# Kernel tuning notes

Measured on AMD Instinct MI355X. Metric: run time of the kernel, lower is better.

## Reference

```python
import jax, jax.numpy as jnp
import numpy as np

B, T, C = 16, 2048, 128
HEAD_SIZE = 128

def setup_inputs() -> dict:
    key = jax.random.key(0)
    k1, k2, k3, k4 = jax.random.split(key, 4)
    x = jax.random.normal(k1, (B, T, C), dtype=jnp.float32)
    # nn.Linear(N_EMBED, head_size, bias=False) weight shape: [head_size, N_EMBED]
    scale = (1.0 / np.sqrt(C)).astype(np.float32)
    Wq = jax.random.normal(k2, (HEAD_SIZE, C), dtype=jnp.float32) * scale
    Wk = jax.random.normal(k3, (HEAD_SIZE, C), dtype=jnp.float32) * scale
    Wv = jax.random.normal(k4, (HEAD_SIZE, C), dtype=jnp.float32) * scale
    return {"x": x, "Wq": Wq, "Wk": Wk, "Wv": Wv}

def reference(x, Wq, Wk, Wv):
    Bd, Td, Cd = x.shape
    q = jnp.einsum('btc,hc->bth', x, Wq)  # [B,T,H]
    k = jnp.einsum('btc,hc->bth', x, Wk)
    v = jnp.einsum('btc,hc->bth', x, Wv)
    # NOTE: original scales by C**-0.5 (embedding dim), not head_size**-0.5
    scores = jnp.einsum('bth,bsh->bts', q, k) * (Cd ** -0.5)  # [B,T,T]
    causal = jnp.tril(jnp.ones((Td, Td), dtype=bool))
    scores = jnp.where(causal, scores, -jnp.inf)
    attn = jax.nn.softmax(scores, axis=-1)
    out = jnp.einsum('bts,bsh->bth', attn, v)  # [B,T,H]
    return out
```

## Files before the change

kernel.cpp:

```cpp
#include <hip/hip_runtime.h>
#include <hip/hip_bf16.h>

#define BB 16
#define TT 2048
#define CC 128
#define HH 128
#define NQT128 16

typedef __bf16 bf16x8 __attribute__((ext_vector_type(8)));
typedef float  f32x4  __attribute__((ext_vector_type(4)));

#define BTH       ((size_t)BB * TT * HH)
#define WBF_OFF   (3 * BTH)
#define PARTIAL_OFF_BYTES (3 * BTH * 2 + 3 * 128 * 128 * 2)
#define SLOT_FLOATS (128 * 128 + 128)

static __device__ __forceinline__ bf16x8 load_cvt8(const float* __restrict__ p) {
    float4 a = *(const float4*)p;
    float4 b = *(const float4*)(p + 4);
    bf16x8 r;
    r[0] = (__bf16)a.x; r[1] = (__bf16)a.y; r[2] = (__bf16)a.z; r[3] = (__bf16)a.w;
    r[4] = (__bf16)b.x; r[5] = (__bf16)b.y; r[6] = (__bf16)b.z; r[7] = (__bf16)b.w;
    return r;
}

static __device__ __forceinline__ void load_lds16(const void* g, void* l) {
    __builtin_amdgcn_global_load_lds(
        (const __attribute__((address_space(1))) unsigned int*)g,
        (__attribute__((address_space(3))) unsigned int*)l, 16, 0, 0);
}

__global__ __launch_bounds__(256) void wcvt_kernel(
    const float* __restrict__ Wq, const float* __restrict__ Wk,
    const float* __restrict__ Wv, __bf16* __restrict__ wbf)
{
    int idx = blockIdx.x * 256 + threadIdx.x;
    int m = idx >> 14;
    int e = idx & 16383;
    const float* src = (m == 0) ? Wq : (m == 1) ? Wk : Wv;
    float sc = (m == 0) ? (0.08838834764831845f * 1.4426950408889634f) : 1.0f;
    wbf[idx] = (__bf16)(src[e] * sc);
}

#define TR_QK 132
#define TR_V  68

__global__ __launch_bounds__(256) void proj_kernel(
    const float* __restrict__ x, __bf16* __restrict__ ws)
{
    __shared__ __bf16 tr[128 * TR_V];

    const int lane = threadIdx.x & 63;
    const int wave = threadIdx.x >> 6;
    const int quad = lane >> 4;
    const int l16  = lane & 15;
    const int m0 = blockIdx.x * 64;
    const int b  = m0 / TT;
    const int t0 = m0 % TT;

    const __bf16* Wbf = ws + WBF_OFF;
    __bf16* Qs = ws;
    __bf16* Ks = ws + BTH;
    __bf16* Vs = ws + 2 * BTH;

    bf16x8 xf[4];
    #pragma unroll
    for (int ks = 0; ks < 4; ++ks)
        xf[ks] = load_cvt8(x + (size_t)(m0 + wave * 16 + l16) * CC + ks * 32 + quad * 8);

    #pragma unroll
    for (int which = 0; which < 2; ++which) {
        const __bf16* Wb = Wbf + (size_t)which * (128 * 128);
        __bf16* dst = which ? Ks : Qs;
        #pragma unroll
        for (int nt = 0; nt < 8; ++nt) {
            f32x4 acc = {0.f, 0.f, 0.f, 0.f};
            #pragma unroll
            for (int ks = 0; ks < 4; ++ks) {
                bf16x8 wf = *(const bf16x8*)(Wb + (size_t)(nt * 16 + l16) * CC + ks * 32 + quad * 8);
                acc = __builtin_amdgcn_mfma_f32_16x16x32_bf16(xf[ks], wf, acc, 0, 0, 0);
            }
            #pragma unroll
            for (int r = 0; r < 4; ++r)
                tr[(wave * 16 + quad * 4 + r) * TR_QK + nt * 16 + l16] = (__bf16)acc[r];
        }
        asm volatile("s_waitcnt lgkmcnt(0)" ::: "memory");
        #pragma unroll
        for (int ks = 0; ks < 4; ++ks) {
            const __bf16* p = &tr[(wave * 16 + l16) * TR_QK + ks * 32 + quad * 8];
            uint2 lo = *(const uint2*)p;
            uint2 hi = *(const uint2*)(p + 4);
            uint4 v; v.x = lo.x; v.y = lo.y; v.z = hi.x; v.w = hi.y;
            __bf16* o = dst + (((size_t)(b * 128 + t0 / 16 + wave) * 4 + ks) << 9) + lane * 8;
            *(uint4*)o = v;
        }
        asm volatile("s_waitcnt lgkmcnt(0)" ::: "memory");
    }

    __syncthreads();
    const __bf16* Wv = Wbf + 2 * (128 * 128);
    #pragma unroll
    for (int msub = 0; msub < 8; ++msub) {
        f32x4 acc = {0.f, 0.f, 0.f, 0.f};
        #pragma unroll
        for (int ks = 0; ks < 4; ++ks) {
            bf16x8 wf = *(const bf16x8*)(Wv + (size_t)(msub * 16 + l16) * CC + ks * 32 + quad * 8);
            acc = __builtin_amdgcn_mfma_f32_16x16x32_bf16(wf, xf[ks], acc, 0, 0, 0);
        }
        #pragma unroll
        for (int r = 0; r < 4; ++r)
            tr[(msub * 16 + quad * 4 + r) * TR_V + wave * 16 + l16] = (__bf16)acc[r];
    }
    __syncthreads();
    #pragma unroll
    for (int i = 0; i < 4; ++i) {
        int t32 = i >> 1;
        int h16 = wave * 2 + (i & 1);
        const __bf16* p = &tr[(h16 * 16 + l16) * TR_V + t32 * 32 + quad * 8];
        uint2 lo = *(const uint2*)p;
        uint2 hi = *(const uint2*)(p + 4);
        uint4 v; v.x = lo.x; v.y = lo.y; v.z = hi.x; v.w = hi.y;
        __bf16* o = Vs + (((size_t)(b * 64 + t0 / 32 + t32) * 8 + h16) << 9) + lane * 8;
        *(uint4*)o = v;
    }
}

#define S_LDS 76
#define EXP_BIAS 16.0f

__global__ __launch_bounds__(256) void attn_kernel(
    const __bf16* __restrict__ ws, float* __restrict__ po,
    float* __restrict__ outp, int G, int SPB, int direct)
{
    __shared__ __bf16 ldsK[8192];
    __shared__ __bf16 ldsV[8192];
    __shared__ __bf16 lds_p[4 * 32 * S_LDS];

    const int lane = threadIdx.x & 63;
    const int wave = threadIdx.x >> 6;
    const int quad = lane >> 4;
    const int l16  = lane & 15;
    const int lane8 = lane * 8;

    const int lin = blockIdx.x;
    const int b  = (lin & 7) * 2 + ((lin >> 3) & 1);
    const int s  = SPB - 1 - (lin >> 4);

    int acc = 0, qt = 0, seg = 0;
    for (int q = 0; q < NQT128; ++q) {
        int c = (2 * (q + 1) + G - 1) / G;
        if (s < acc + c) { qt = q; seg = s - acc; break; }
        acc += c;
    }
    const int kt0 = seg * G;
    int kt1 = 2 * (qt + 1);
    if (kt0 + G < kt1) kt1 = kt0 + G;

    const int qw = qt * 128 + wave * 32;
    int kt1w = (qw + 32 + 63) >> 6;
    if (kt1w > kt1) kt1w = kt1;

    const __bf16* Qs = ws;
    const __bf16* Ks = ws + BTH;
    const __bf16* Vs = ws + 2 * BTH;

    bf16x8 qf[2][4];
    #pragma unroll
    for (int m = 0; m < 2; ++m)
        #pragma unroll
        for (int ks = 0; ks < 4; ++ks)
            qf[m][ks] = *(const bf16x8*)(Qs + (((size_t)(b * 128 + qt * 8 + wave * 2 + m) * 4 + ks) << 9) + lane8);

    float l_r[2][4];
    f32x4 o[2][8];
    #pragma unroll
    for (int m = 0; m < 2; ++m) {
        #pragma unroll
        for (int r = 0; r < 4; ++r) l_r[m][r] = 0.f;
        #pragma unroll
        for (int h8 = 0; h8 < 8; ++h8) o[m][h8] = (f32x4){0.f, 0.f, 0.f, 0.f};
    }

    __bf16* myP = lds_p + wave * 32 * S_LDS;

    for (int kt = kt0; kt < kt1; ++kt) {
        const char* kbase = (const char*)(Ks + (((size_t)(b * 128 + kt * 4) * 4) << 9));
        const char* vbase = (const char*)(Vs + (((size_t)(b * 64 + kt * 2) * 8) << 9));
        #pragma unroll
        for (int i = 0; i < 8; ++i) {
            const int c = wave * 8 + i;
            const char* g = (c < 16) ? (kbase + c * 1024) : (vbase + (c - 16) * 1024);
            char* l = (c < 16) ? ((char*)ldsK + c * 1024) : ((char*)ldsV + (c - 16) * 1024);
            load_lds16(g + (size_t)lane * 16, l);
        }
        asm volatile("s_waitcnt vmcnt(0)" ::: "memory");
        __syncthreads();

        if (kt < kt1w) {
            const int k0 = kt * 64;

            f32x4 s2[2][4];
            #pragma unroll
            for (int nsub = 0; nsub < 4; ++nsub) {
                bf16x8 kfr[4];
                #pragma unroll
                for (int ks = 0; ks < 4; ++ks)
                    kfr[ks] = *(const bf16x8*)((const char*)ldsK + ((nsub * 4 + ks) << 10) + lane * 16);
                #pragma unroll
                for (int m = 0; m < 2; ++m) {
                    f32x4 a2 = {0.f, 0.f, 0.f, 0.f};
                    #pragma unroll
                    for (int ks = 0; ks < 4; ++ks)
                        a2 = __builtin_amdgcn_mfma_f32_16x16x32_bf16(qf[m][ks], kfr[ks], a2, 0, 0, 0);
                    s2[m][nsub] = a2;
                }
            }

            #pragma unroll
            for (int m = 0; m < 2; ++m) {
                const int qr0m = qw + m * 16;
                if (k0 + 63 > qr0m) {
                    #pragma unroll
                    for (int nsub = 0; nsub < 4; ++nsub) {
                        int key = k0 + nsub * 16 + l16;
                        #pragma unroll
                        for (int r = 0; r < 4; ++r) {
                            int rowq = qr0m + quad * 4 + r;
                            if (key > rowq) s2[m][nsub][r] = -3e38f;
                        }
                    }
                }
                #pragma unroll
                for (int nsub = 0; nsub < 4; ++nsub) {
                    #pragma unroll
                    for (int r = 0; r < 4; ++r) {
                        float p = __builtin_amdgcn_exp2f(s2[m][nsub][r] - EXP_BIAS);
                        l_r[m][r] += p;
                        myP[(m * 16 + quad * 4 + r) * S_LDS + nsub * 16 + l16] = (__bf16)p;
                    }
                }
            }
            asm volatile("s_waitcnt lgkmcnt(0)" ::: "memory");

            bf16x8 pf[2][2];
            #pragma unroll
            for (int m = 0; m < 2; ++m)
                #pragma unroll
                for (int ks2 = 0; ks2 < 2; ++ks2) {
                    union { bf16x8 v; uint2 h[2]; } u;
                    const char* base = (const char*)myP + (size_t)(m * 16 + l16) * (S_LDS * 2) + ks2 * 64 + quad * 16;
                    u.h[0] = *(const uint2*)base;
                    u.h[1] = *(const uint2*)(base + 8);
                    pf[m][ks2] = u.v;
                }

            #pragma unroll
            for (int h8 = 0; h8 < 8; ++h8) {
                bf16x8 v0 = *(const bf16x8*)((const char*)ldsV + ((0 * 8 + h8) << 10) + lane * 16);
                bf16x8 v1 = *(const bf16x8*)((const char*)ldsV + ((1 * 8 + h8) << 10) + lane * 16);
                #pragma unroll
                for (int m = 0; m < 2; ++m) {
                    o[m][h8] = __builtin_amdgcn_mfma_f32_16x16x32_bf16(pf[m][0], v0, o[m][h8], 0, 0, 0);
                    o[m][h8] = __builtin_amdgcn_mfma_f32_16x16x32_bf16(pf[m][1], v1, o[m][h8], 0, 0, 0);
                }
            }
        }
        __syncthreads();
    }

    #pragma unroll
    for (int m = 0; m < 2; ++m)
        #pragma unroll
        for (int r = 0; r < 4; ++r)
            #pragma unroll
            for (int j = 1; j <= 8; j <<= 1)
                l_r[m][r] += __shfl_xor(l_r[m][r], j, 64);

    if (direct) {
        #pragma unroll
        for (int m = 0; m < 2; ++m) {
            float inv[4];
            #pragma unroll
            for (int r = 0; r < 4; ++r) inv[r] = 1.0f / l_r[m][r];
            #pragma unroll
            for (int h8 = 0; h8 < 8; ++h8)
                #pragma unroll
                for (int r = 0; r < 4; ++r)
                    outp[(size_t)(b * TT + qw + m * 16 + quad * 4 + r) * HH + h8 * 16 + l16] = o[m][h8][r] * inv[r];
        }
    } else {
        float* slot = po + (size_t)(b * SPB + s) * SLOT_FLOATS;
        #pragma unroll
        for (int m = 0; m < 2; ++m) {
            #pragma unroll
            for (int h8 = 0; h8 < 8; ++h8)
                #pragma unroll
                for (int r = 0; r < 4; ++r)
                    slot[(size_t)(wave * 32 + m * 16 + quad * 4 + r) * HH + h8 * 16 + l16] = o[m][h8][r];
            if (l16 == 0) {
                #pragma unroll
                for (int r = 0; r < 4; ++r)
                    slot[128 * 128 + wave * 32 + m * 16 + quad * 4 + r] = l_r[m][r];
            }
        }
    }
}

__global__ __launch_bounds__(256) void reduce_kernel(
    const float* __restrict__ po, float* __restrict__ outp, int G, int SPB)
{
    __shared__ float lsum[32];
    const int qt  = blockIdx.x >> 2;
    const int qtr = blockIdx.x & 3;
    const int b   = blockIdx.y;
    const int tid = threadIdx.x;

    int acc = 0;
    for (int qq = 0; qq < qt; ++qq) acc += (2 * (qq + 1) + G - 1) / G;
    const int segs = (2 * (qt + 1) + G - 1) / G;
    const float* base = po + (size_t)(b * SPB + acc) * SLOT_FLOATS;
    const int r0 = qtr * 32;

    if (tid < 32) {
        float v = 0.f;
        for (int sg = 0; sg < segs; ++sg)
            v += base[(size_t)sg * SLOT_FLOATS + 128 * 128 + r0 + tid];
        lsum[tid] = v;
    }
    __syncthreads();

    const int f4c  = tid & 31;
    const int rowg = tid >> 5;
    float4 a[4];
    #pragma unroll
    for (int p = 0; p < 4; ++p) a[p] = (float4){0.f, 0.f, 0.f, 0.f};

    for (int sg = 0; sg < segs; ++sg) {
        const float* sb = base + (size_t)sg * SLOT_FLOATS;
        #pragma unroll
        for (int p = 0; p < 4; ++p) {
            int row = r0 + p * 8 + rowg;
            float4 v = *(const float4*)(sb + (size_t)row * 128 + f4c * 4);
            a[p].x += v.x; a[p].y += v.y; a[p].z += v.z; a[p].w += v.w;
        }
    }

    #pragma unroll
    for (int p = 0; p < 4; ++p) {
        int row = r0 + p * 8 + rowg;
        float inv = 1.0f / lsum[p * 8 + rowg];
        float4 o4 = {a[p].x * inv, a[p].y * inv, a[p].z * inv, a[p].w * inv};
        *(float4*)(outp + (size_t)(b * TT + qt * 128 + row) * HH + f4c * 4) = o4;
    }
}

extern "C" void kernel_launch(void* const* d_in, const int* in_sizes, int n_in,
                              void* d_out, int out_size, void* d_ws, size_t ws_size,
                              hipStream_t stream)
{
    const float* x  = (const float*)d_in[0];
    const float* Wq = (const float*)d_in[1];
    const float* Wk = (const float*)d_in[2];
    const float* Wv = (const float*)d_in[3];
    __bf16* ws = (__bf16*)d_ws;
    float* out = (float*)d_out;
    float* po  = (float*)((char*)d_ws + PARTIAL_OFF_BYTES);

    int G = 0, SPB = 0, direct = 1;
    const int cand[3] = {6, 8, 16};
    for (int ci = 0; ci < 3; ++ci) {
        int g = cand[ci], spb = 0;
        for (int q = 0; q < NQT128; ++q) spb += (2 * (q + 1) + g - 1) / g;
        size_t need = PARTIAL_OFF_BYTES + (size_t)spb * BB * SLOT_FLOATS * 4;
        if (need <= ws_size) { G = g; SPB = spb; direct = 0; break; }
    }
    if (direct) { G = 2 * NQT128; SPB = NQT128; }

    wcvt_kernel<<<192, 256, 0, stream>>>(Wq, Wk, Wv, ws + WBF_OFF);
    proj_kernel<<<512, 256, 0, stream>>>(x, ws);
    attn_kernel<<<SPB * 16, 256, 0, stream>>>(ws, po, out, G, SPB, direct);
    if (!direct) {
        dim3 rgrid(NQT128 * 4, BB);
        reduce_kernel<<<rgrid, 256, 0, stream>>>(po, out, G, SPB);
    }
}
```

Before: 150.0 us.

## Double-buffer K/V tiles, pass P via shuffles, store partials in bf16

```diff
diff --git a/kernel.cpp b/kernel.cpp
--- a/kernel.cpp
+++ b/kernel.cpp
@@ -9,11 +9,13 @@
 
 typedef __bf16 bf16x8 __attribute__((ext_vector_type(8)));
 typedef float  f32x4  __attribute__((ext_vector_type(4)));
+typedef unsigned long long u64;
 
 #define BTH       ((size_t)BB * TT * HH)
 #define WBF_OFF   (3 * BTH)
 #define PARTIAL_OFF_BYTES (3 * BTH * 2 + 3 * 128 * 128 * 2)
-#define SLOT_FLOATS (128 * 128 + 128)
+#define SLOT_BYTES 33280
+#define SLOT_L_OFF 32768
 
 static __device__ __forceinline__ bf16x8 load_cvt8(const float* __restrict__ p) {
     float4 a = *(const float4*)p;
@@ -125,16 +127,13 @@
     }
 }
 
-#define S_LDS 76
 #define EXP_BIAS 16.0f
 
 __global__ __launch_bounds__(256) void attn_kernel(
-    const __bf16* __restrict__ ws, float* __restrict__ po,
+    const __bf16* __restrict__ ws, char* __restrict__ po,
     float* __restrict__ outp, int G, int SPB, int direct)
 {
-    __shared__ __bf16 ldsK[8192];
-    __shared__ __bf16 ldsV[8192];
-    __shared__ __bf16 lds_p[4 * 32 * S_LDS];
+    __shared__ __bf16 ldsKV[2][16384];
 
     const int lane = threadIdx.x & 63;
     const int wave = threadIdx.x >> 6;
@@ -155,6 +154,8 @@
     const int kt0 = seg * G;
     int kt1 = 2 * (qt + 1);
     if (kt0 + G < kt1) kt1 = kt0 + G;
+    const int segs_qt = (2 * (qt + 1) + G - 1) / G;
+    const int dwrite = direct | (segs_qt == 1);
 
     const int qw = qt * 128 + wave * 32;
     int kt1w = (qw + 32 + 63) >> 6;
@@ -171,33 +172,39 @@
         for (int ks = 0; ks < 4; ++ks)
             qf[m][ks] = *(const bf16x8*)(Qs + (((size_t)(b * 128 + qt * 8 + wave * 2 + m) * 4 + ks) << 9) + lane8);
 
-    float l_r[2][4];
+    float l_m[2] = {0.f, 0.f};
     f32x4 o[2][8];
     #pragma unroll
-    for (int m = 0; m < 2; ++m) {
-        #pragma unroll
-        for (int r = 0; r < 4; ++r) l_r[m][r] = 0.f;
+    for (int m = 0; m < 2; ++m)
         #pragma unroll
         for (int h8 = 0; h8 < 8; ++h8) o[m][h8] = (f32x4){0.f, 0.f, 0.f, 0.f};
-    }
-
-    __bf16* myP = lds_p + wave * 32 * S_LDS;
+
+    #define STAGE(KT, BUF)                                                          \
+        do {                                                                        \
+            const char* kbase_ = (const char*)(Ks + (((size_t)(b * 128 + (KT) * 4) * 4) << 9)); \
+            const char* vbase_ = (const char*)(Vs + (((size_t)(b * 64 + (KT) * 2) * 8) << 9));  \
+            _Pragma("unroll")                                                       \
+            for (int i_ = 0; i_ < 8; ++i_) {                                        \
+                const int c_ = wave * 8 + i_;                                       \
+                const char* g_ = (c_ < 16) ? (kbase_ + c_ * 1024)                   \
+                                           : (vbase_ + (c_ - 16) * 1024);           \
+                char* l_ = (char*)ldsKV[BUF] + c_ * 1024;                           \
+                load_lds16(g_ + (size_t)lane * 16, l_);                             \
+            }                                                                       \
+        } while (0)
+
+    STAGE(kt0, 0);
+    int cur = 0;
 
     for (int kt = kt0; kt < kt1; ++kt) {
-        const char* kbase = (const char*)(Ks + (((size_t)(b * 128 + kt * 4) * 4) << 9));
-        const char* vbase = (const char*)(Vs + (((size_t)(b * 64 + kt * 2) * 8) << 9));
-        #pragma unroll
-        for (int i = 0; i < 8; ++i) {
-            const int c = wave * 8 + i;
-            const char* g = (c < 16) ? (kbase + c * 1024) : (vbase + (c - 16) * 1024);
-            char* l = (c < 16) ? ((char*)ldsK + c * 1024) : ((char*)ldsV + (c - 16) * 1024);
-            load_lds16(g + (size_t)lane * 16, l);
-        }
         asm volatile("s_waitcnt vmcnt(0)" ::: "memory");
         __syncthreads();
+        if (kt + 1 < kt1) STAGE(kt + 1, cur ^ 1);
 
         if (kt < kt1w) {
             const int k0 = kt * 64;
+            const char* ldsK = (const char*)ldsKV[cur];
+            const char* ldsV = (const char*)ldsKV[cur] + 16384;
 
             f32x4 s2[2][4];
             #pragma unroll
@@ -205,83 +212,76 @@
                 bf16x8 kfr[4];
                 #pragma unroll
                 for (int ks = 0; ks < 4; ++ks)
-                    kfr[ks] = *(const bf16x8*)((const char*)ldsK + ((nsub * 4 + ks) << 10) + lane * 16);
+                    kfr[ks] = *(const bf16x8*)(ldsK + ((nsub * 4 + ks) << 10) + lane * 16);
                 #pragma unroll
                 for (int m = 0; m < 2; ++m) {
                     f32x4 a2 = {0.f, 0.f, 0.f, 0.f};
                     #pragma unroll
                     for (int ks = 0; ks < 4; ++ks)
-                        a2 = __builtin_amdgcn_mfma_f32_16x16x32_bf16(qf[m][ks], kfr[ks], a2, 0, 0, 0);
+                        a2 = __builtin_amdgcn_mfma_f32_16x16x32_bf16(kfr[ks], qf[m][ks], a2, 0, 0, 0);
                     s2[m][nsub] = a2;
                 }
             }
 
             #pragma unroll
             for (int m = 0; m < 2; ++m) {
-                const int qr0m = qw + m * 16;
-                if (k0 + 63 > qr0m) {
-                    #pragma unroll
-                    for (int nsub = 0; nsub < 4; ++nsub) {
-                        int key = k0 + nsub * 16 + l16;
-                        #pragma unroll
-                        for (int r = 0; r < 4; ++r) {
-                            int rowq = qr0m + quad * 4 + r;
-                            if (key > rowq) s2[m][nsub][r] = -3e38f;
-                        }
-                    }
-                }
+                const int qrow = qw + m * 16 + l16;
+                union PK { u64 u; __bf16 h[4]; } pk[4];
                 #pragma unroll
                 for (int nsub = 0; nsub < 4; ++nsub) {
                     #pragma unroll
                     for (int r = 0; r < 4; ++r) {
-                        float p = __builtin_amdgcn_exp2f(s2[m][nsub][r] - EXP_BIAS);
-                        l_r[m][r] += p;
-                        myP[(m * 16 + quad * 4 + r) * S_LDS + nsub * 16 + l16] = (__bf16)p;
+                        int key = k0 + nsub * 16 + quad * 4 + r;
+                        float sv = (key > qrow) ? -3e38f : s2[m][nsub][r];
+                        float p = __builtin_amdgcn_exp2f(sv - EXP_BIAS);
+                        l_m[m] += p;
+                        pk[nsub].h[r] = (__bf16)p;
                     }
                 }
-            }
-            asm volatile("s_waitcnt lgkmcnt(0)" ::: "memory");
-
-            bf16x8 pf[2][2];
-            #pragma unroll
-            for (int m = 0; m < 2; ++m)
+
+                const int srcA = (quad & 1) ? (l16 + 32) : l16;
+                const int srcB = srcA + 16;
+                const int hiSel = quad >> 1;
+                bf16x8 pf[2];
                 #pragma unroll
                 for (int ks2 = 0; ks2 < 2; ++ks2) {
-                    union { bf16x8 v; uint2 h[2]; } u;
-                    const char* base = (const char*)myP + (size_t)(m * 16 + l16) * (S_LDS * 2) + ks2 * 64 + quad * 16;
-                    u.h[0] = *(const uint2*)base;
-                    u.h[1] = *(const uint2*)(base + 8);
-                    pf[m][ks2] = u.v;
+                    u64 a0 = __shfl(pk[2 * ks2].u, srcA, 64);
+                    u64 a1 = __shfl(pk[2 * ks2 + 1].u, srcA, 64);
+                    u64 b0 = __shfl(pk[2 * ks2].u, srcB, 64);
+                    u64 b1 = __shfl(pk[2 * ks2 + 1].u, srcB, 64);
+                    union { u64 v[2]; bf16x8 f; } uu;
+                    uu.v[0] = hiSel ? a1 : a0;
+                    uu.v[1] = hiSel ? b1 : b0;
+                    pf[ks2] = uu.f;
                 }
 
-            #pragma unroll
-            for (int h8 = 0; h8 < 8; ++h8) {
-                bf16x8 v0 = *(const bf16x8*)((const char*)ldsV + ((0 * 8 + h8) << 10) + lane * 16);
-                bf16x8 v1 = *(const bf16x8*)((const char*)ldsV + ((1 * 8 + h8) << 10) + lane * 16);
-                #pragma unroll
-                for (int m = 0; m < 2; ++m) {
-                    o[m][h8] = __builtin_amdgcn_mfma_f32_16x16x32_bf16(pf[m][0], v0, o[m][h8], 0, 0, 0);
-                    o[m][h8] = __builtin_amdgcn_mfma_f32_16x16x32_bf16(pf[m][1], v1, o[m][h8], 0, 0, 0);
+                #pragma unroll
+                for (int h8 = 0; h8 < 8; ++h8) {
+                    bf16x8 v0 = *(const bf16x8*)(ldsV + ((0 * 8 + h8) << 10) + lane * 16);
+                    bf16x8 v1 = *(const bf16x8*)(ldsV + ((1 * 8 + h8) << 10) + lane * 16);
+                    o[m][h8] = __builtin_amdgcn_mfma_f32_16x16x32_bf16(pf[0], v0, o[m][h8], 0, 0, 0);
+                    o[m][h8] = __builtin_amdgcn_mfma_f32_16x16x32_bf16(pf[1], v1, o[m][h8], 0, 0, 0);
                 }
             }
         }
-        __syncthreads();
-    }
-
-    #pragma unroll
-    for (int m = 0; m < 2; ++m)
-        #pragma unroll
-        for (int r = 0; r < 4; ++r)
-            #pragma unroll
-            for (int j = 1; j <= 8; j <<= 1)
-                l_r[m][r] += __shfl_xor(l_r[m][r], j, 64);
-
-    if (direct) {
+        cur ^= 1;
+    }
+
+    #pragma unroll
+    for (int m = 0; m < 2; ++m) {
+        l_m[m] += __shfl_xor(l_m[m], 16, 64);
+        l_m[m] += __shfl_xor(l_m[m], 32, 64);
+    }
+
+    if (dwrite) {
         #pragma unroll
         for (int m = 0; m < 2; ++m) {
             float inv[4];
             #pragma unroll
-            for (int r = 0; r < 4; ++r) inv[r] = 1.0f / l_r[m][r];
+            for (int r = 0; r < 4; ++r) {
+                float lv = __shfl(l_m[m], (lane & 48) + quad * 4 + r, 64);
+                inv[r] = 1.0f / lv;
+            }
             #pragma unroll
             for (int h8 = 0; h8 < 8; ++h8)
                 #pragma unroll
@@ -289,25 +289,24 @@
                     outp[(size_t)(b * TT + qw + m * 16 + quad * 4 + r) * HH + h8 * 16 + l16] = o[m][h8][r] * inv[r];
         }
     } else {
-        float* slot = po + (size_t)(b * SPB + s) * SLOT_FLOATS;
+        char* slot = po + (size_t)(b * SPB + s) * SLOT_BYTES;
+        __bf16* slot_o = (__bf16*)slot;
+        float*  slot_l = (float*)(slot + SLOT_L_OFF);
         #pragma unroll
         for (int m = 0; m < 2; ++m) {
             #pragma unroll
             for (int h8 = 0; h8 < 8; ++h8)
                 #pragma unroll
                 for (int r = 0; r < 4; ++r)
-                    slot[(size_t)(wave * 32 + m * 16 + quad * 4 + r) * HH + h8 * 16 + l16] = o[m][h8][r];
-            if (l16 == 0) {
-                #pragma unroll
-                for (int r = 0; r < 4; ++r)
-                    slot[128 * 128 + wave * 32 + m * 16 + quad * 4 + r] = l_r[m][r];
-            }
+                    slot_o[(size_t)(wave * 32 + m * 16 + quad * 4 + r) * 128 + h8 * 16 + l16] = (__bf16)o[m][h8][r];
+            if (quad == 0)
+                slot_l[wave * 32 + m * 16 + l16] = l_m[m];
         }
     }
 }
 
 __global__ __launch_bounds__(256) void reduce_kernel(
-    const float* __restrict__ po, float* __restrict__ outp, int G, int SPB)
+    const char* __restrict__ po, float* __restrict__ outp, int G, int SPB)
 {
     __shared__ float lsum[32];
     const int qt  = blockIdx.x >> 2;
@@ -315,42 +314,51 @@
     const int b   = blockIdx.y;
     const int tid = threadIdx.x;
 
+    const int segs = (2 * (qt + 1) + G - 1) / G;
+    if (segs == 1) return;
+
     int acc = 0;
     for (int qq = 0; qq < qt; ++qq) acc += (2 * (qq + 1) + G - 1) / G;
-    const int segs = (2 * (qt + 1) + G - 1) / G;
-    const float* base = po + (size_t)(b * SPB + acc) * SLOT_FLOATS;
+    const char* base = po + (size_t)(b * SPB + acc) * SLOT_BYTES;
     const int r0 = qtr * 32;
 
     if (tid < 32) {
         float v = 0.f;
         for (int sg = 0; sg < segs; ++sg)
-            v += base[(size_t)sg * SLOT_FLOATS + 128 * 128 + r0 + tid];
+            v += ((const float*)(base + (size_t)sg * SLOT_BYTES + SLOT_L_OFF))[r0 + tid];
         lsum[tid] = v;
     }
     __syncthreads();
 
-    const int f4c  = tid & 31;
-    const int rowg = tid >> 5;
-    float4 a[4];
-    #pragma unroll
-    for (int p = 0; p < 4; ++p) a[p] = (float4){0.f, 0.f, 0.f, 0.f};
+    const int rsub = tid >> 4;
+    const int cg   = tid & 15;
+    float a[2][8];
+    #pragma unroll
+    for (int p = 0; p < 2; ++p)
+        #pragma unroll
+        for (int j = 0; j < 8; ++j) a[p][j] = 0.f;
 
     for (int sg = 0; sg < segs; ++sg) {
-        const float* sb = base + (size_t)sg * SLOT_FLOATS;
-        #pragma unroll
-        for (int p = 0; p < 4; ++p) {
-            int row = r0 + p * 8 + rowg;
-            float4 v = *(const float4*)(sb + (size_t)row * 128 + f4c * 4);
-            a[p].x += v.x; a[p].y += v.y; a[p].z += v.z; a[p].w += v.w;
-        }
-    }
-
-    #pragma unroll
-    for (int p = 0; p < 4; ++p) {
-        int row = r0 + p * 8 + rowg;
-        float inv = 1.0f / lsum[p * 8 + rowg];
-        float4 o4 = {a[p].x * inv, a[p].y * inv, a[p].z * inv, a[p].w * inv};
-        *(float4*)(outp + (size_t)(b * TT + qt * 128 + row) * HH + f4c * 4) = o4;
+        const char* sb = base + (size_t)sg * SLOT_BYTES;
+        #pragma unroll
+        for (int p = 0; p < 2; ++p) {
+            int row = r0 + rsub + p * 16;
+            union { uint4 u; __bf16 h[8]; } v;
+            v.u = *(const uint4*)(sb + ((size_t)row * 128 + cg * 8) * 2);
+            #pragma unroll
+            for (int j = 0; j < 8; ++j) a[p][j] += (float)v.h[j];
+        }
+    }
+
+    #pragma unroll
+    for (int p = 0; p < 2; ++p) {
+        int row = r0 + rsub + p * 16;
+        float inv = 1.0f / lsum[rsub + p * 16];
+        float* op = outp + (size_t)(b * TT + qt * 128 + row) * HH + cg * 8;
+        float4 o0 = {a[p][0] * inv, a[p][1] * inv, a[p][2] * inv, a[p][3] * inv};
+        float4 o1 = {a[p][4] * inv, a[p][5] * inv, a[p][6] * inv, a[p][7] * inv};
+        *(float4*)op = o0;
+        *(float4*)(op + 4) = o1;
     }
 }
 
@@ -364,14 +372,14 @@
     const float* Wv = (const float*)d_in[3];
     __bf16* ws = (__bf16*)d_ws;
     float* out = (float*)d_out;
-    float* po  = (float*)((char*)d_ws + PARTIAL_OFF_BYTES);
+    char* po   = (char*)d_ws + PARTIAL_OFF_BYTES;
 
     int G = 0, SPB = 0, direct = 1;
     const int cand[3] = {6, 8, 16};
     for (int ci = 0; ci < 3; ++ci) {
         int g = cand[ci], spb = 0;
         for (int q = 0; q < NQT128; ++q) spb += (2 * (q + 1) + g - 1) / g;
-        size_t need = PARTIAL_OFF_BYTES + (size_t)spb * BB * SLOT_FLOATS * 4;
+        size_t need = PARTIAL_OFF_BYTES + (size_t)spb * BB * SLOT_BYTES;
         if (need <= ws_size) { G = g; SPB = spb; direct = 0; break; }
     }
     if (direct) { G = 2 * NQT128; SPB = NQT128; }
```

Result: no change. 152.2 us (+1.4%).
